# Kernel tuning notes

Hardware: AMD Instinct MI355X
Metric: run time of the kernel (lower is better)

The kernel has to match this reference:

```python
import jax, jax.numpy as jnp
import numpy as np

H = 32  # hidden/input size fixed by the module

def _rnn_layer(x, W_ih, b_ih, W_hh, b_hh):
    # x: [B, T, H]. PyTorch RNN: h_t = tanh(x_t @ W_ih^T + b_ih + h_{t-1} @ W_hh^T + b_hh)
    B = x.shape[0]
    # precompute input projection for all timesteps (one big GEMM)
    xin = jnp.einsum('bth,ih->bti', x, W_ih) + (b_ih + b_hh)  # [B, T, H]
    def step(h, xt):
        h_new = jnp.tanh(xt + h @ W_hh.T)
        return h_new, h_new
    h0 = jnp.zeros((B, H), dtype=x.dtype)
    _, hs = jax.lax.scan(step, h0, jnp.swapaxes(xin, 0, 1))  # hs: [T, B, H]
    return jnp.swapaxes(hs, 0, 1)  # [B, T, H]


def setup_inputs() -> dict:
    key = jax.random.key(0)
    ks = jax.random.split(key, 11)
    s = 1.0 / np.sqrt(H)
    u = lambda k, shape: jax.random.uniform(k, shape, jnp.float32, -s, s)
    x = jax.random.normal(ks[0], (4096, 512, H), dtype=jnp.float32)
    return {
        'x': x,
        'W_ih1': u(ks[1], (H, H)), 'W_hh1': u(ks[2], (H, H)),
        'b_ih1': u(ks[3], (H,)),   'b_hh1': u(ks[4], (H,)),
        'W_ih2': u(ks[5], (H, H)), 'W_hh2': u(ks[6], (H, H)),
        'b_ih2': u(ks[7], (H,)),   'b_hh2': u(ks[8], (H,)),
        'W_fc': u(ks[9], (1, H)),  'b_fc': u(ks[10], (1,)),
    }


def reference(x, W_ih1, W_hh1, b_ih1, b_hh1, W_ih2, W_hh2, b_ih2, b_hh2, W_fc, b_fc):
    h1 = _rnn_layer(x, W_ih1, b_ih1, W_hh1, b_hh1)   # [B, T, H]
    h2 = _rnn_layer(h1, W_ih2, b_ih2, W_hh2, b_hh2)  # [B, T, H]
    last = h2[:, -1, :]                               # [B, H]
    return last @ W_fc.T + b_fc                       # [B, 1]
```

## Files before the change

### kernel.cpp

```cpp
#include <hip/hip_runtime.h>

#define HH 32
#define TT 512
#define CHUNK 8
#define NCHUNK (TT / CHUNK)

__device__ __forceinline__ float fast_tanh(float z) {
    float e, r;
    float zz = z * 2.88539008177793f;
    asm("v_exp_f32 %0, %1" : "=v"(e) : "v"(zz));
    float d = e + 1.0f;
    asm("v_rcp_f32 %0, %1" : "=v"(r) : "v"(d));
    return __builtin_fmaf(-2.0f, r, 1.0f);
}

__global__ void __launch_bounds__(64) __attribute__((amdgpu_waves_per_eu(2, 2)))
rnn_fused(
    const float* __restrict__ x,
    const float* __restrict__ Wih1, const float* __restrict__ Whh1,
    const float* __restrict__ bih1, const float* __restrict__ bhh1,
    const float* __restrict__ Wih2, const float* __restrict__ Whh2,
    const float* __restrict__ bih2, const float* __restrict__ bhh2,
    const float* __restrict__ Wfc, const float* __restrict__ bfc,
    float* __restrict__ out)
{
    __shared__ __align__(16) float x_lds[2][CHUNK * HH];
    __shared__ __align__(16) float h1_lds[2][HH];
    __shared__ __align__(16) float h2_lds[2][HH];

    const int lane = threadIdx.x;
    const int g = lane >> 5;
    const int i = lane & 31;
    const int b = blockIdx.x * 2 + g;

    float4 w1[8], u1[8], w2[8], u2[8];
#pragma unroll
    for (int q = 0; q < 8; ++q) {
        w1[q] = ((const float4*)(Wih1 + i * HH))[q];
        u1[q] = ((const float4*)(Whh1 + i * HH))[q];
        w2[q] = ((const float4*)(Wih2 + i * HH))[q];
        u2[q] = ((const float4*)(Whh2 + i * HH))[q];
    }
    const float bias1 = bih1[i] + bhh1[i];
    const float bias2 = bih2[i] + bhh2[i];
    const float wfc = Wfc[i];

    const float* xb = x + (size_t)b * (TT * HH);

    float4 r0 = ((const float4*)xb)[i];
    float4 r1 = ((const float4*)xb)[i + 32];

    float4 h1r[8];
#pragma unroll
    for (int j = 0; j < 8; ++j) h1r[j] = make_float4(0.f, 0.f, 0.f, 0.f);
    float h2_own = 0.0f;
    h2_lds[g][i] = 0.0f;

    float4* xl4 = (float4*)&x_lds[g][0];
    const float4* h1l4 = (const float4*)&h1_lds[g][0];
    const float4* h2l4 = (const float4*)&h2_lds[g][0];

    for (int c = 0; c < NCHUNK; ++c) {
        xl4[i] = r0;
        xl4[i + 32] = r1;
        asm volatile("s_waitcnt lgkmcnt(0)" ::: "memory");
        {
            const int cn = (c + 1 < NCHUNK) ? c + 1 : c;
            const float4* src = (const float4*)(xb + cn * (CHUNK * HH));
            r0 = src[i];
            r1 = src[i + 32];
        }
#pragma unroll
        for (int s = 0; s < CHUNK; ++s) {
            float p0 = bias1, p1 = 0.f, p2 = 0.f, p3 = 0.f;
#pragma unroll
            for (int j = 0; j < 8; ++j) {
                float4 xv = xl4[s * 8 + j];
                p0 = __builtin_fmaf(w1[j].x, xv.x, p0);
                p1 = __builtin_fmaf(w1[j].y, xv.y, p1);
                p2 = __builtin_fmaf(w1[j].z, xv.z, p2);
                p3 = __builtin_fmaf(w1[j].w, xv.w, p3);
            }
#pragma unroll
            for (int j = 0; j < 8; ++j) {
                p0 = __builtin_fmaf(u1[j].x, h1r[j].x, p0);
                p1 = __builtin_fmaf(u1[j].y, h1r[j].y, p1);
                p2 = __builtin_fmaf(u1[j].z, h1r[j].z, p2);
                p3 = __builtin_fmaf(u1[j].w, h1r[j].w, p3);
            }
            float h1n = fast_tanh((p0 + p1) + (p2 + p3));
            h1_lds[g][i] = h1n;
            asm volatile("s_waitcnt lgkmcnt(0)" ::: "memory");

            float q0 = bias2, q1 = 0.f, q2 = 0.f, q3 = 0.f;
#pragma unroll
            for (int j = 0; j < 8; ++j) {
                float4 h1v = h1l4[j];
                float4 h2v = h2l4[j];
                h1r[j] = h1v;
                q0 = __builtin_fmaf(w2[j].x, h1v.x, q0);
                q1 = __builtin_fmaf(w2[j].y, h1v.y, q1);
                q2 = __builtin_fmaf(w2[j].z, h1v.z, q2);
                q3 = __builtin_fmaf(w2[j].w, h1v.w, q3);
                q0 = __builtin_fmaf(u2[j].x, h2v.x, q0);
                q1 = __builtin_fmaf(u2[j].y, h2v.y, q1);
                q2 = __builtin_fmaf(u2[j].z, h2v.z, q2);
                q3 = __builtin_fmaf(u2[j].w, h2v.w, q3);
            }
            float h2n = fast_tanh((q0 + q1) + (q2 + q3));
            h2_own = h2n;
            h2_lds[g][i] = h2n;
        }
    }

    h1_lds[g][i] = h2_own * wfc;
    asm volatile("s_waitcnt lgkmcnt(0)" ::: "memory");
    if (i == 0) {
        float sacc = bfc[0];
#pragma unroll
        for (int j = 0; j < HH; ++j) sacc += h1_lds[g][j];
        out[b] = sacc;
    }
}

extern "C" void kernel_launch(void* const* d_in, const int* in_sizes, int n_in,
                              void* d_out, int out_size, void* d_ws, size_t ws_size,
                              hipStream_t stream) {
    const float* x    = (const float*)d_in[0];
    const float* Wih1 = (const float*)d_in[1];
    const float* Whh1 = (const float*)d_in[2];
    const float* bih1 = (const float*)d_in[3];
    const float* bhh1 = (const float*)d_in[4];
    const float* Wih2 = (const float*)d_in[5];
    const float* Whh2 = (const float*)d_in[6];
    const float* bih2 = (const float*)d_in[7];
    const float* bhh2 = (const float*)d_in[8];
    const float* Wfc  = (const float*)d_in[9];
    const float* bfc  = (const float*)d_in[10];
    float* out = (float*)d_out;

    rnn_fused<<<dim3(2048), dim3(64), 0, stream>>>(
        x, Wih1, Whh1, bih1, bhh1, Wih2, Whh2, bih2, bhh2, Wfc, bfc, out);
}
```

Baseline: 556.3 us.

## Rewrite RNN kernel as one wave per sequence with DPP matvec and skewed layers

Each 64-lane wave now handles one batch row. The low 32 lanes compute layer 1 and the high 32 lanes compute layer 2, skewed by one timestep so both layers advance in a single phase. Matrix-vector products use inline-asm v_fmac with DPP row_ror rotations over pre-rotated per-lane weights, ds_bpermute replaces the LDS round trips for broadcasting hidden state, and x is prefetched straight into registers. Blocks grow to 128 threads with waves_per_eu 4. This targets LDS latency and the serial two-layer dependency per step, at the cost of fragile inline asm, more registers, and duplicated lane work.

```diff
diff --git a/kernel.cpp b/kernel.cpp
--- a/kernel.cpp
+++ b/kernel.cpp
@@ -1,9 +1,6 @@
 #include <hip/hip_runtime.h>
 
-#define HH 32
 #define TT 512
-#define CHUNK 8
-#define NCHUNK (TT / CHUNK)
 
 __device__ __forceinline__ float fast_tanh(float z) {
     float e, r;
@@ -14,8 +11,32 @@
     return __builtin_fmaf(-2.0f, r, 1.0f);
 }
 
-__global__ void __launch_bounds__(64) __attribute__((amdgpu_waves_per_eu(2, 2)))
-rnn_fused(
+__device__ __forceinline__ float chain16(float acc, float o, const float* w) {
+    asm("s_nop 1\n\t"
+        "v_fmac_f32 %0, %1, %2  row_ror:1  row_mask:0xf bank_mask:0xf\n\t"
+        "v_fmac_f32 %0, %1, %3  row_ror:2  row_mask:0xf bank_mask:0xf\n\t"
+        "v_fmac_f32 %0, %1, %4  row_ror:3  row_mask:0xf bank_mask:0xf\n\t"
+        "v_fmac_f32 %0, %1, %5  row_ror:4  row_mask:0xf bank_mask:0xf\n\t"
+        "v_fmac_f32 %0, %1, %6  row_ror:5  row_mask:0xf bank_mask:0xf\n\t"
+        "v_fmac_f32 %0, %1, %7  row_ror:6  row_mask:0xf bank_mask:0xf\n\t"
+        "v_fmac_f32 %0, %1, %8  row_ror:7  row_mask:0xf bank_mask:0xf\n\t"
+        "v_fmac_f32 %0, %1, %9  row_ror:8  row_mask:0xf bank_mask:0xf\n\t"
+        "v_fmac_f32 %0, %1, %10 row_ror:9  row_mask:0xf bank_mask:0xf\n\t"
+        "v_fmac_f32 %0, %1, %11 row_ror:10 row_mask:0xf bank_mask:0xf\n\t"
+        "v_fmac_f32 %0, %1, %12 row_ror:11 row_mask:0xf bank_mask:0xf\n\t"
+        "v_fmac_f32 %0, %1, %13 row_ror:12 row_mask:0xf bank_mask:0xf\n\t"
+        "v_fmac_f32 %0, %1, %14 row_ror:13 row_mask:0xf bank_mask:0xf\n\t"
+        "v_fmac_f32 %0, %1, %15 row_ror:14 row_mask:0xf bank_mask:0xf\n\t"
+        "v_fmac_f32 %0, %1, %16 row_ror:15 row_mask:0xf bank_mask:0xf"
+        : "+v"(acc)
+        : "v"(o), "v"(w[1]), "v"(w[2]), "v"(w[3]), "v"(w[4]), "v"(w[5]),
+          "v"(w[6]), "v"(w[7]), "v"(w[8]), "v"(w[9]), "v"(w[10]), "v"(w[11]),
+          "v"(w[12]), "v"(w[13]), "v"(w[14]), "v"(w[15]));
+    return acc;
+}
+
+__global__ void __launch_bounds__(128) __attribute__((amdgpu_waves_per_eu(4, 4)))
+rnn_dpp(
     const float* __restrict__ x,
     const float* __restrict__ Wih1, const float* __restrict__ Whh1,
     const float* __restrict__ bih1, const float* __restrict__ bhh1,
@@ -24,103 +45,88 @@
     const float* __restrict__ Wfc, const float* __restrict__ bfc,
     float* __restrict__ out)
 {
-    __shared__ __align__(16) float x_lds[2][CHUNK * HH];
-    __shared__ __align__(16) float h1_lds[2][HH];
-    __shared__ __align__(16) float h2_lds[2][HH];
+    const int L = threadIdx.x & 63;
+    const int b = blockIdx.x * 2 + (threadIdx.x >> 6);
+    const int r = L & 15;
+    const bool lo32 = (L < 32);
+    const int out_row = ((L >> 4) & 1) * 16 + r;
 
-    const int lane = threadIdx.x;
-    const int g = lane >> 5;
-    const int i = lane & 31;
-    const int b = blockIdx.x * 2 + g;
+    const float* WA = lo32 ? Wih1 : Wih2;
+    const float* WB = lo32 ? Whh1 : Whh2;
+    float w0[16], w1[16], w2[16], w3[16];
+#pragma unroll
+    for (int k = 0; k < 16; ++k) {
+        int jlo = (r - k) & 15;
+        w0[k] = WA[out_row * 32 + jlo];
+        w1[k] = WA[out_row * 32 + 16 + jlo];
+        w2[k] = WB[out_row * 32 + jlo];
+        w3[k] = WB[out_row * 32 + 16 + jlo];
+    }
+    const float biasv = lo32 ? (bih1[out_row] + bhh1[out_row])
+                             : (bih2[out_row] + bhh2[out_row]);
 
-    float4 w1[8], u1[8], w2[8], u2[8];
+    const int idx_plo = 4 * r;
+    const int idx_phi = 4 * (16 | r);
+    const int idx_s2  = 4 * ((L & 32) | r);
+    const int idx_s3  = 4 * ((L & 32) | 16 | r);
+
+    const float* xb = x + (size_t)b * (TT * 32);
+
+    float myh = 0.0f;
+
+    auto phase = [&](float xlo, float xhi) {
+        int mh = __float_as_int(myh);
+        float Plo = __int_as_float(__builtin_amdgcn_ds_bpermute(idx_plo, mh));
+        float Phi = __int_as_float(__builtin_amdgcn_ds_bpermute(idx_phi, mh));
+        float S2  = __int_as_float(__builtin_amdgcn_ds_bpermute(idx_s2, mh));
+        float S3  = __int_as_float(__builtin_amdgcn_ds_bpermute(idx_s3, mh));
+        float S0 = lo32 ? xlo : Plo;
+        float S1 = lo32 ? xhi : Phi;
+        float a0 = __builtin_fmaf(S0, w0[0], biasv);
+        float a1 = S1 * w1[0];
+        float a2 = S2 * w2[0];
+        float a3 = S3 * w3[0];
+        a0 = chain16(a0, S0, w0);
+        a1 = chain16(a1, S1, w1);
+        a2 = chain16(a2, S2, w2);
+        a3 = chain16(a3, S3, w3);
+        myh = fast_tanh((a0 + a1) + (a2 + a3));
+    };
+
+    float xp[2][8];
 #pragma unroll
-    for (int q = 0; q < 8; ++q) {
-        w1[q] = ((const float4*)(Wih1 + i * HH))[q];
-        u1[q] = ((const float4*)(Whh1 + i * HH))[q];
-        w2[q] = ((const float4*)(Wih2 + i * HH))[q];
-        u2[q] = ((const float4*)(Whh2 + i * HH))[q];
+    for (int s = 0; s < 4; ++s) {
+        xp[0][2 * s]     = xb[s * 32 + r];
+        xp[0][2 * s + 1] = xb[s * 32 + 16 + r];
     }
-    const float bias1 = bih1[i] + bhh1[i];
-    const float bias2 = bih2[i] + bhh2[i];
-    const float wfc = Wfc[i];
 
-    const float* xb = x + (size_t)b * (TT * HH);
-
-    float4 r0 = ((const float4*)xb)[i];
-    float4 r1 = ((const float4*)xb)[i + 32];
-
-    float4 h1r[8];
+#pragma unroll 2
+    for (int c = 0; c < 128; ++c) {
+        const int cp = (c + 1 < 128) ? c + 1 : 127;
 #pragma unroll
-    for (int j = 0; j < 8; ++j) h1r[j] = make_float4(0.f, 0.f, 0.f, 0.f);
-    float h2_own = 0.0f;
-    h2_lds[g][i] = 0.0f;
-
-    float4* xl4 = (float4*)&x_lds[g][0];
-    const float4* h1l4 = (const float4*)&h1_lds[g][0];
-    const float4* h2l4 = (const float4*)&h2_lds[g][0];
-
-    for (int c = 0; c < NCHUNK; ++c) {
-        xl4[i] = r0;
-        xl4[i + 32] = r1;
-        asm volatile("s_waitcnt lgkmcnt(0)" ::: "memory");
-        {
-            const int cn = (c + 1 < NCHUNK) ? c + 1 : c;
-            const float4* src = (const float4*)(xb + cn * (CHUNK * HH));
-            r0 = src[i];
-            r1 = src[i + 32];
+        for (int s = 0; s < 4; ++s) {
+            xp[(c + 1) & 1][2 * s]     = xb[(cp * 4 + s) * 32 + r];
+            xp[(c + 1) & 1][2 * s + 1] = xb[(cp * 4 + s) * 32 + 16 + r];
         }
 #pragma unroll
-        for (int s = 0; s < CHUNK; ++s) {
-            float p0 = bias1, p1 = 0.f, p2 = 0.f, p3 = 0.f;
-#pragma unroll
-            for (int j = 0; j < 8; ++j) {
-                float4 xv = xl4[s * 8 + j];
-                p0 = __builtin_fmaf(w1[j].x, xv.x, p0);
-                p1 = __builtin_fmaf(w1[j].y, xv.y, p1);
-                p2 = __builtin_fmaf(w1[j].z, xv.z, p2);
-                p3 = __builtin_fmaf(w1[j].w, xv.w, p3);
+        for (int s = 0; s < 4; ++s) {
+            phase(xp[c & 1][2 * s], xp[c & 1][2 * s + 1]);
+            if (c == 0 && s == 0) {
+                myh = lo32 ? myh : 0.0f;
             }
-#pragma unroll
-            for (int j = 0; j < 8; ++j) {
-                p0 = __builtin_fmaf(u1[j].x, h1r[j].x, p0);
-                p1 = __builtin_fmaf(u1[j].y, h1r[j].y, p1);
-                p2 = __builtin_fmaf(u1[j].z, h1r[j].z, p2);
-                p3 = __builtin_fmaf(u1[j].w, h1r[j].w, p3);
-            }
-            float h1n = fast_tanh((p0 + p1) + (p2 + p3));
-            h1_lds[g][i] = h1n;
-            asm volatile("s_waitcnt lgkmcnt(0)" ::: "memory");
-
-            float q0 = bias2, q1 = 0.f, q2 = 0.f, q3 = 0.f;
-#pragma unroll
-            for (int j = 0; j < 8; ++j) {
-                float4 h1v = h1l4[j];
-                float4 h2v = h2l4[j];
-                h1r[j] = h1v;
-                q0 = __builtin_fmaf(w2[j].x, h1v.x, q0);
-                q1 = __builtin_fmaf(w2[j].y, h1v.y, q1);
-                q2 = __builtin_fmaf(w2[j].z, h1v.z, q2);
-                q3 = __builtin_fmaf(w2[j].w, h1v.w, q3);
-                q0 = __builtin_fmaf(u2[j].x, h2v.x, q0);
-                q1 = __builtin_fmaf(u2[j].y, h2v.y, q1);
-                q2 = __builtin_fmaf(u2[j].z, h2v.z, q2);
-                q3 = __builtin_fmaf(u2[j].w, h2v.w, q3);
-            }
-            float h2n = fast_tanh((q0 + q1) + (q2 + q3));
-            h2_own = h2n;
-            h2_lds[g][i] = h2n;
         }
     }
+    phase(xp[0][0], xp[0][1]);
 
-    h1_lds[g][i] = h2_own * wfc;
-    asm volatile("s_waitcnt lgkmcnt(0)" ::: "memory");
-    if (i == 0) {
-        float sacc = bfc[0];
-#pragma unroll
-        for (int j = 0; j < HH; ++j) sacc += h1_lds[g][j];
-        out[b] = sacc;
-    }
+    float wfcv = Wfc[L & 31];
+    float rr = lo32 ? 0.0f : myh * wfcv;
+    rr += __shfl_xor(rr, 1);
+    rr += __shfl_xor(rr, 2);
+    rr += __shfl_xor(rr, 4);
+    rr += __shfl_xor(rr, 8);
+    rr += __shfl_xor(rr, 16);
+    rr += __shfl_xor(rr, 32);
+    if (L == 0) out[b] = rr + bfc[0];
 }
 
 extern "C" void kernel_launch(void* const* d_in, const int* in_sizes, int n_in,
@@ -139,6 +145,6 @@
     const float* bfc  = (const float*)d_in[10];
     float* out = (float*)d_out;
 
-    rnn_fused<<<dim3(2048), dim3(64), 0, stream>>>(
+    rnn_dpp<<<dim3(2048), dim3(128), 0, stream>>>(
         x, Wih1, Whh1, bih1, bhh1, Wih2, Whh2, bih2, bhh2, Wfc, bfc, out);
 }
```

Measured after the change: 574.2 us. 3.2% more time.
